# Optimization experiments

Measured on AMD Instinct MI355X. Metric: run time of the kernel, lower is better.

## Reference

```python
import jax, jax.numpy as jnp
import numpy as np

N_NODES = 100000
N_EDGES = 600000
N_GRAPHS = 64


def _segment_mean(x, seg_ids, num_segments):
    s = jax.ops.segment_sum(x, seg_ids, num_segments=num_segments)
    cnt = jax.ops.segment_sum(jnp.ones((x.shape[0],), x.dtype), seg_ids, num_segments=num_segments)
    return s / jnp.maximum(cnt, 1.0)[:, None]


def _sage_conv(x, src, dst, W_l, W_r, b):
    # PyG SAGEConv (mean aggr): out = lin_l(mean_{j->i} x_j) + lin_r(x_i)
    mean_nb = _segment_mean(x[src], dst, x.shape[0])  # [N, d_in]
    return mean_nb @ W_l.T + x @ W_r.T + b


def setup_inputs() -> dict:
    key = jax.random.key(0)
    ks = jax.random.split(key, 16)
    bert_cls = jax.random.normal(ks[0], (N_GRAPHS, 768), jnp.float32)
    node_x = jax.random.normal(ks[1], (N_NODES, 128), jnp.float32)
    edge_index = jax.random.randint(ks[2], (2, N_EDGES), 0, N_NODES, jnp.int64 if jax.config.jax_enable_x64 else jnp.int32)
    batch_ids = jnp.sort(jax.random.randint(ks[3], (N_NODES,), 0, N_GRAPHS))
    s = 0.05
    return {
        'bert_cls': bert_cls,
        'node_x': node_x,
        'edge_index': edge_index,
        'batch_ids': batch_ids,
        'W_adapt': jax.random.normal(ks[4], (64, 768), jnp.float32) * s,
        'b_adapt': jnp.zeros((64,), jnp.float32),
        'W1l': jax.random.normal(ks[5], (64, 128), jnp.float32) * s,
        'W1r': jax.random.normal(ks[6], (64, 128), jnp.float32) * s,
        'b1': jnp.zeros((64,), jnp.float32),
        'W2l': jax.random.normal(ks[7], (16, 64), jnp.float32) * s,
        'W2r': jax.random.normal(ks[8], (16, 64), jnp.float32) * s,
        'b2': jnp.zeros((16,), jnp.float32),
        'Wm': jax.random.normal(ks[9], (16, 16), jnp.float32) * s,
        'bm': jnp.zeros((16,), jnp.float32),
    }


def reference(bert_cls, node_x, edge_index, batch_ids,
              W_adapt, b_adapt, W1l, W1r, b1, W2l, W2r, b2, Wm, bm):
    # pooled BERT CLS -> adaptive linear (forward() applies no relu here)
    last_state = bert_cls @ W_adapt.T + b_adapt  # [bs, 64]

    src, dst = edge_index[0], edge_index[1]
    h = jax.nn.relu(_sage_conv(node_x, src, dst, W1l, W1r, b1))  # [N, 64]
    h = _sage_conv(h, src, dst, W2l, W2r, b2)                    # [N, 16]

    graph_emb = _segment_mean(h, batch_ids, N_GRAPHS)            # [bs, 16]
    graph_emb = graph_emb @ Wm.T + bm

    return jnp.concatenate([last_state, graph_emb], axis=-1)     # [bs, 80]
```

## Files before the change

kernel.cpp:

```cpp
#include <hip/hip_runtime.h>

#define N_NODES 100000
#define N_EDGES 600000
#define N_GRAPHS 64


__global__ void k_count(const int* __restrict__ dst, int* __restrict__ deg) {
    int e = blockIdx.x * 256 + threadIdx.x;
    if (e < N_EDGES) atomicAdd(&deg[dst[e]], 1);
}

__global__ void k_scan1(const int* __restrict__ deg, int* __restrict__ offs,
                        int* __restrict__ bsums) {
    __shared__ int s[256];
    int t = threadIdx.x, b = blockIdx.x;
    int base = b * 1024 + t * 4;
    int v0 = (base + 0 < N_NODES) ? deg[base + 0] : 0;
    int v1 = (base + 1 < N_NODES) ? deg[base + 1] : 0;
    int v2 = (base + 2 < N_NODES) ? deg[base + 2] : 0;
    int v3 = (base + 3 < N_NODES) ? deg[base + 3] : 0;
    int tsum = v0 + v1 + v2 + v3;
    s[t] = tsum;
    __syncthreads();
    for (int o = 1; o < 256; o <<= 1) {
        int x = (t >= o) ? s[t - o] : 0;
        __syncthreads();
        s[t] += x;
        __syncthreads();
    }
    int p = s[t] - tsum;
    if (base + 0 < N_NODES) offs[base + 0] = p;
    p += v0;
    if (base + 1 < N_NODES) offs[base + 1] = p;
    p += v1;
    if (base + 2 < N_NODES) offs[base + 2] = p;
    p += v2;
    if (base + 3 < N_NODES) offs[base + 3] = p;
    if (t == 255) bsums[b] = s[255];
}

__global__ void k_scan2(const int* __restrict__ bsums, int* __restrict__ boff) {
    __shared__ int s[128];
    int t = threadIdx.x;
    int nb = (N_NODES + 1023) / 1024;
    int v = (t < nb) ? bsums[t] : 0;
    s[t] = v;
    __syncthreads();
    for (int o = 1; o < 128; o <<= 1) {
        int x = (t >= o) ? s[t - o] : 0;
        __syncthreads();
        s[t] += x;
        __syncthreads();
    }
    boff[t] = s[t] - v;
}

__global__ void k_scan3(int* __restrict__ offs, const int* __restrict__ boff,
                        int* __restrict__ cursor) {
    int i = blockIdx.x * 256 + threadIdx.x;
    if (i < N_NODES) {
        int v = offs[i] + boff[i >> 10];
        offs[i] = v;
        cursor[i] = v;
    }
}

__global__ void k_fill(const int* __restrict__ src, const int* __restrict__ dst,
                       int* __restrict__ cursor, int* __restrict__ ssrc) {
    int e = blockIdx.x * 256 + threadIdx.x;
    if (e < N_EDGES) {
        int d = dst[e];
        int pos = atomicAdd(&cursor[d], 1);
        ssrc[pos] = src[e];
    }
}

__global__ void k_prepack(const float* __restrict__ W1l, const float* __restrict__ W1r,
                          const float* __restrict__ W2l, const float* __restrict__ W2r,
                          float* __restrict__ Pg, float2* __restrict__ P2) {
    int i = blockIdx.x * 256 + threadIdx.x;
    if (i < 16384) {
        int k = i >> 7, d = i & 127;
        Pg[i] = (d < 64) ? W1l[d * 128 + k] : W1r[(d - 64) * 128 + k];
    } else if (i < 16896) {
        int j = i - 16384, m = j >> 4, d = j & 15;
        P2[j] = make_float2(W2l[d * 64 + 2 * m], W2l[d * 64 + 2 * m + 1]);
    } else if (i < 17408) {
        int j = i - 16896, m = j >> 4, d = j & 15;
        P2[512 + j] = make_float2(W2r[d * 64 + 2 * m], W2r[d * 64 + 2 * m + 1]);
    }
}


#define KC 32
#define LDP 132

__launch_bounds__(256, 4)
__global__ void k_xform1(const float* __restrict__ x, const float* __restrict__ Pg,
                         float* __restrict__ xl, float* __restrict__ xr) {
    __shared__ float At[KC * LDP];
    __shared__ float Bt[KC * LDP];
    int tid = threadIdx.x;
    int wave = tid >> 6, lane = tid & 63;
    int wr = wave >> 1, wc = wave & 1;
    int li = lane >> 3, lj = lane & 7;
    int tbase = blockIdx.x * 128;
    const float4* x4 = (const float4*)x;
    const float4* Pg4 = (const float4*)Pg;

    float acc[8][8];
#pragma unroll
    for (int i = 0; i < 8; ++i)
#pragma unroll
        for (int j = 0; j < 8; ++j) acc[i][j] = 0.f;

    for (int k0 = 0; k0 < 128; k0 += KC) {
        if (k0) __syncthreads();
#pragma unroll
        for (int u = 0; u < 4; ++u) {
            int idx = u * 256 + tid;
            int n = idx >> 3, q = idx & 7;
            int node = min(tbase + n, N_NODES - 1);
            float4 v = x4[node * 32 + (k0 >> 2) + q];
            At[(4 * q + 0) * LDP + n] = v.x;
            At[(4 * q + 1) * LDP + n] = v.y;
            At[(4 * q + 2) * LDP + n] = v.z;
            At[(4 * q + 3) * LDP + n] = v.w;
        }
#pragma unroll
        for (int u = 0; u < 4; ++u) {
            int idx = u * 256 + tid;
            int kk = idx >> 5, q = idx & 31;
            float4 w = Pg4[(k0 + kk) * 32 + q];
            *(float4*)&Bt[kk * LDP + 4 * q] = w;
        }
        __syncthreads();
#pragma unroll 4
        for (int kk = 0; kk < KC; ++kk) {
            float a[8], b[8];
            *(float4*)&a[0] = *(const float4*)&At[kk * LDP + wr * 64 + li * 8];
            *(float4*)&a[4] = *(const float4*)&At[kk * LDP + wr * 64 + li * 8 + 4];
            *(float4*)&b[0] = *(const float4*)&Bt[kk * LDP + wc * 64 + lj * 8];
            *(float4*)&b[4] = *(const float4*)&Bt[kk * LDP + wc * 64 + lj * 8 + 4];
#pragma unroll
            for (int i = 0; i < 8; ++i)
#pragma unroll
                for (int j = 0; j < 8; ++j)
                    acc[i][j] = fmaf(a[i], b[j], acc[i][j]);
        }
    }
    float* outb = wc ? xr : xl;
#pragma unroll
    for (int i = 0; i < 8; ++i) {
        int node = tbase + wr * 64 + li * 8 + i;
        if (node < N_NODES) {
            float4* p = (float4*)(outb + node * 64 + lj * 8);
            p[0] = make_float4(acc[i][0], acc[i][1], acc[i][2], acc[i][3]);
            p[1] = make_float4(acc[i][4], acc[i][5], acc[i][6], acc[i][7]);
        }
    }
}


__launch_bounds__(256)
__global__ void k_gather1(const float* __restrict__ xl, const int* __restrict__ ssrc,
                          const int* __restrict__ offs, const int* __restrict__ deg,
                          const float* __restrict__ b1, float* __restrict__ h1) {
    int tid = blockIdx.x * 256 + threadIdx.x;
    int wid = tid >> 6, lane = tid & 63;
    int nWaves = (gridDim.x * 256) >> 6;
    float bias = b1[lane];

    for (int node = wid; node < N_NODES; node += nWaves) {
        int o  = __builtin_amdgcn_readfirstlane(offs[node]);
        int dg = __builtin_amdgcn_readfirstlane(deg[node]);
        float self = h1[node * 64 + lane];
        float a0 = 0.f, a1 = 0.f, a2 = 0.f, a3 = 0.f;
        int last = dg - 1;
        for (int u = 0; u < dg; u += 4) {
            int n0 = ssrc[o + u];
            int n1 = ssrc[o + min(u + 1, last)];
            int n2 = ssrc[o + min(u + 2, last)];
            int n3 = ssrc[o + min(u + 3, last)];
            float v0 = xl[n0 * 64 + lane];
            float v1 = xl[n1 * 64 + lane];
            float v2 = xl[n2 * 64 + lane];
            float v3 = xl[n3 * 64 + lane];
            float m1 = (u + 1 < dg) ? 1.f : 0.f;
            float m2 = (u + 2 < dg) ? 1.f : 0.f;
            float m3 = (u + 3 < dg) ? 1.f : 0.f;
            a0 += v0;
            a1 = fmaf(v1, m1, a1);
            a2 = fmaf(v2, m2, a2);
            a3 = fmaf(v3, m3, a3);
        }
        float inv = 1.f / (float)max(dg, 1);
        h1[node * 64 + lane] = fmaxf(self + bias + ((a0 + a1) + (a2 + a3)) * inv, 0.f);
    }
}


__launch_bounds__(256)
__global__ void k_xform2(const float* __restrict__ h1,
                         const float2* __restrict__ Pl, const float2* __restrict__ Pr,
                         float* __restrict__ h1l, float* __restrict__ h2pre) {
    __shared__ float2 S[64 * 32];
    int tid = threadIdx.x;
    int wave = __builtin_amdgcn_readfirstlane(tid >> 6);
    int lane = tid & 63;
    int tbase = blockIdx.x * 64;
    const float4* h4 = (const float4*)h1;

    for (int idx = tid; idx < 64 * 16; idx += 256) {
        int n = idx >> 4, m4 = idx & 15;
        if (tbase + n < N_NODES) {
            float4 v = h4[(tbase + n) * 16 + m4];
            int swz = n & 31;
            S[n * 32 + ((2 * m4) ^ swz)]     = make_float2(v.x, v.y);
            S[n * 32 + ((2 * m4 + 1) ^ swz)] = make_float2(v.z, v.w);
        }
    }
    __syncthreads();

    int node = tbase + lane;
    int dbase = wave * 4;
    float accl[4] = {0.f, 0.f, 0.f, 0.f};
    float accr[4] = {0.f, 0.f, 0.f, 0.f};
    int swz = lane & 31;
    const float2* Sn = S + lane * 32;
#pragma unroll 4
    for (int m = 0; m < 32; ++m) {
        float2 s = Sn[m ^ swz];
        const float2* Wl = Pl + m * 16 + dbase;
        const float2* Wr = Pr + m * 16 + dbase;
#pragma unroll
        for (int dd = 0; dd < 4; ++dd) {
            accl[dd] = fmaf(Wl[dd].x, s.x, fmaf(Wl[dd].y, s.y, accl[dd]));
            accr[dd] = fmaf(Wr[dd].x, s.x, fmaf(Wr[dd].y, s.y, accr[dd]));
        }
    }
    if (node < N_NODES) {
        *(float4*)(h1l + node * 16 + dbase)   = make_float4(accl[0], accl[1], accl[2], accl[3]);
        *(float4*)(h2pre + node * 16 + dbase) = make_float4(accr[0], accr[1], accr[2], accr[3]);
    }
}


__launch_bounds__(256)
__global__ void k_g2pool(const float* __restrict__ h1l, const float* __restrict__ h2pre,
                         const int* __restrict__ ssrc, const int* __restrict__ offs,
                         const int* __restrict__ deg, const int* __restrict__ batch,
                         const float* __restrict__ b2,
                         float* __restrict__ gsum, float* __restrict__ gcnt) {
    __shared__ float bins[N_GRAPHS][17];
    int tid = threadIdx.x;
    for (int i = tid; i < N_GRAPHS * 17; i += 256) ((float*)bins)[i] = 0.f;
    __syncthreads();

    int wave = tid >> 6, lane = tid & 63;
    int sub = lane >> 4, d = lane & 15;
    float bias = b2[d];

    int chunk = (N_NODES + gridDim.x - 1) / gridDim.x;
    int cs = blockIdx.x * chunk;
    int ce = min(N_NODES, cs + chunk);

    for (int base = cs + wave * 4; base < ce; base += 16) {
        int node = base + sub;
        bool valid = node < ce;
        int nn = valid ? node : cs;
        int o = offs[nn], dg = deg[nn];
        float a0 = 0.f, a1 = 0.f, a2 = 0.f, a3 = 0.f;
        int last = dg - 1;
        for (int u = 0; u < dg; u += 4) {
            int n0 = ssrc[o + u];
            int n1 = ssrc[o + min(u + 1, last)];
            int n2 = ssrc[o + min(u + 2, last)];
            int n3 = ssrc[o + min(u + 3, last)];
            float v0 = h1l[n0 * 16 + d];
            float v1 = h1l[n1 * 16 + d];
            float v2 = h1l[n2 * 16 + d];
            float v3 = h1l[n3 * 16 + d];
            float m1 = (u + 1 < dg) ? 1.f : 0.f;
            float m2 = (u + 2 < dg) ? 1.f : 0.f;
            float m3 = (u + 3 < dg) ? 1.f : 0.f;
            a0 += v0;
            a1 = fmaf(v1, m1, a1);
            a2 = fmaf(v2, m2, a2);
            a3 = fmaf(v3, m3, a3);
        }
        float inv = 1.f / (float)max(dg, 1);
        float val = h2pre[nn * 16 + d] + bias + ((a0 + a1) + (a2 + a3)) * inv;
        if (valid) {
            int g = batch[nn];
            atomicAdd(&bins[g][d], val);
            if (d == 0) atomicAdd(&bins[g][16], 1.f);
        }
    }
    __syncthreads();
    for (int i = tid; i < N_GRAPHS * 17; i += 256) {
        int g = i / 17, c = i - g * 17;
        float v = bins[g][c];
        if (v != 0.f) {
            if (c < 16) atomicAdd(&gsum[g * 16 + c], v);
            else        atomicAdd(&gcnt[g], v);
        }
    }
}


__global__ void k_final(const float* __restrict__ bert, const float* __restrict__ Wad,
                        const float* __restrict__ bad, const float* __restrict__ Wm,
                        const float* __restrict__ bm, const float* __restrict__ gsum,
                        const float* __restrict__ gcnt, float* __restrict__ out) {
    int g = blockIdx.x;
    int t = threadIdx.x;
    if (t < 64) {
        const float4* br = (const float4*)(bert + g * 768);
        const float4* wr = (const float4*)(Wad + t * 768);
        float acc = bad[t];
#pragma unroll 8
        for (int k = 0; k < 192; ++k) {
            float4 bv = br[k], wv = wr[k];
            acc += bv.x * wv.x + bv.y * wv.y + bv.z * wv.z + bv.w * wv.w;
        }
        out[g * 80 + t] = acc;
    } else if (t < 80) {
        int j = t - 64;
        float ic = 1.f / fmaxf(gcnt[g], 1.f);
        float acc = bm[j];
#pragma unroll
        for (int k = 0; k < 16; ++k) acc += Wm[j * 16 + k] * gsum[g * 16 + k] * ic;
        out[g * 80 + t] = acc;
    }
}

extern "C" void kernel_launch(void* const* d_in, const int* in_sizes, int n_in,
                              void* d_out, int out_size, void* d_ws, size_t ws_size,
                              hipStream_t stream) {
    const float* bert   = (const float*)d_in[0];
    const float* node_x = (const float*)d_in[1];
    const int*   edge   = (const int*)d_in[2];
    const int*   batch  = (const int*)d_in[3];
    const float* Wad    = (const float*)d_in[4];
    const float* bad    = (const float*)d_in[5];
    const float* W1l    = (const float*)d_in[6];
    const float* W1r    = (const float*)d_in[7];
    const float* b1     = (const float*)d_in[8];
    const float* W2l    = (const float*)d_in[9];
    const float* W2r    = (const float*)d_in[10];
    const float* b2     = (const float*)d_in[11];
    const float* Wm     = (const float*)d_in[12];
    const float* bm     = (const float*)d_in[13];
    float* out = (float*)d_out;

    const int* src = edge;
    const int* dst = edge + N_EDGES;

    char* ws = (char*)d_ws;
    int*    deg    = (int*)(ws);
    int*    offs   = (int*)(ws + 400000);
    int*    cursor = (int*)(ws + 800000);
    int*    bsums  = (int*)(ws + 1200000);
    int*    boff   = (int*)(ws + 1200512);
    int*    ssrc   = (int*)(ws + 1201024);
    float*  xl     = (float*)(ws + 3601024);
    float*  h1     = (float*)(ws + 29201024);
    float*  Pg     = (float*)(ws + 54801024);
    float2* P2     = (float2*)(ws + 54866560);
    float*  gsum   = (float*)(ws + 54874752);
    float*  gcnt   = (float*)(ws + 54878848);
    float*  h1l    = (float*)(ws + 3601024);
    float*  h2pre  = (float*)(ws + 10001024);

    float2* P2l = P2;
    float2* P2r = P2 + 512;

    hipMemsetAsync(deg, 0, 400000, stream);
    hipMemsetAsync(gsum, 0, 4096 + 256, stream);

    k_count<<<(N_EDGES + 255) / 256, 256, 0, stream>>>(dst, deg);
    k_scan1<<<(N_NODES + 1023) / 1024, 256, 0, stream>>>(deg, offs, bsums);
    k_scan2<<<1, 128, 0, stream>>>(bsums, boff);
    k_scan3<<<(N_NODES + 255) / 256, 256, 0, stream>>>(offs, boff, cursor);
    k_fill<<<(N_EDGES + 255) / 256, 256, 0, stream>>>(src, dst, cursor, ssrc);
    k_prepack<<<68, 256, 0, stream>>>(W1l, W1r, W2l, W2r, Pg, P2);

    int nT128 = (N_NODES + 127) / 128;
    int nT64  = (N_NODES + 63) / 64;
    k_xform1<<<nT128, 256, 0, stream>>>(node_x, Pg, xl, h1);
    k_gather1<<<2048, 256, 0, stream>>>(xl, ssrc, offs, deg, b1, h1);
    k_xform2<<<nT64, 256, 0, stream>>>(h1, P2l, P2r, h1l, h2pre);
    k_g2pool<<<512, 256, 0, stream>>>(h1l, h2pre, ssrc, offs, deg, batch, b2, gsum, gcnt);
    k_final<<<N_GRAPHS, 128, 0, stream>>>(bert, Wad, bad, Wm, bm, gsum, gcnt, out);
}
```

Before: 325.2 us.

## Prefetch GEMM tiles, swizzle LDS, unroll gather by 8, restructure layer-2 transform

```diff
diff --git a/kernel.cpp b/kernel.cpp
--- a/kernel.cpp
+++ b/kernel.cpp
@@ -77,17 +77,14 @@
 
 __global__ void k_prepack(const float* __restrict__ W1l, const float* __restrict__ W1r,
                           const float* __restrict__ W2l, const float* __restrict__ W2r,
-                          float* __restrict__ Pg, float2* __restrict__ P2) {
+                          float* __restrict__ Pg, float* __restrict__ P2g) {
     int i = blockIdx.x * 256 + threadIdx.x;
     if (i < 16384) {
         int k = i >> 7, d = i & 127;
         Pg[i] = (d < 64) ? W1l[d * 128 + k] : W1r[(d - 64) * 128 + k];
-    } else if (i < 16896) {
-        int j = i - 16384, m = j >> 4, d = j & 15;
-        P2[j] = make_float2(W2l[d * 64 + 2 * m], W2l[d * 64 + 2 * m + 1]);
-    } else if (i < 17408) {
-        int j = i - 16896, m = j >> 4, d = j & 15;
-        P2[512 + j] = make_float2(W2r[d * 64 + 2 * m], W2r[d * 64 + 2 * m + 1]);
+    } else if (i < 18432) {
+        int j = i - 16384, k = j >> 5, d = j & 31;
+        P2g[j] = (d < 16) ? W2l[d * 64 + k] : W2r[(d - 16) * 64 + k];
     }
 }
 
@@ -108,6 +105,15 @@
     const float4* x4 = (const float4*)x;
     const float4* Pg4 = (const float4*)Pg;
 
+    float4 av[4], bv[4];
+#pragma unroll
+    for (int u = 0; u < 4; ++u) {
+        int idx = u * 256 + tid;
+        int n = idx >> 3, q = idx & 7;
+        int node = min(tbase + n, N_NODES - 1);
+        av[u] = x4[node * 32 + q];
+        bv[u] = Pg4[idx];
+    }
     float acc[8][8];
 #pragma unroll
     for (int i = 0; i < 8; ++i)
@@ -115,31 +121,35 @@
         for (int j = 0; j < 8; ++j) acc[i][j] = 0.f;
 
     for (int k0 = 0; k0 < 128; k0 += KC) {
-        if (k0) __syncthreads();
 #pragma unroll
         for (int u = 0; u < 4; ++u) {
             int idx = u * 256 + tid;
             int n = idx >> 3, q = idx & 7;
-            int node = min(tbase + n, N_NODES - 1);
-            float4 v = x4[node * 32 + (k0 >> 2) + q];
-            At[(4 * q + 0) * LDP + n] = v.x;
-            At[(4 * q + 1) * LDP + n] = v.y;
-            At[(4 * q + 2) * LDP + n] = v.z;
-            At[(4 * q + 3) * LDP + n] = v.w;
-        }
-#pragma unroll
-        for (int u = 0; u < 4; ++u) {
-            int idx = u * 256 + tid;
-            int kk = idx >> 5, q = idx & 31;
-            float4 w = Pg4[(k0 + kk) * 32 + q];
-            *(float4*)&Bt[kk * LDP + 4 * q] = w;
-        }
-        __syncthreads();
+            int ns = n ^ ((q & 7) << 3);
+            At[(4 * q + 0) * LDP + ns] = av[u].x;
+            At[(4 * q + 1) * LDP + ns] = av[u].y;
+            At[(4 * q + 2) * LDP + ns] = av[u].z;
+            At[(4 * q + 3) * LDP + ns] = av[u].w;
+            int kk = idx >> 5, q2 = idx & 31;
+            *(float4*)&Bt[kk * LDP + 4 * q2] = bv[u];
+        }
+        __syncthreads();
+        if (k0 + KC < 128) {
+#pragma unroll
+            for (int u = 0; u < 4; ++u) {
+                int idx = u * 256 + tid;
+                int n = idx >> 3, q = idx & 7;
+                int node = min(tbase + n, N_NODES - 1);
+                av[u] = x4[node * 32 + ((k0 + KC) >> 2) + q];
+                bv[u] = Pg4[(k0 + KC) * 32 + idx];
+            }
+        }
 #pragma unroll 4
         for (int kk = 0; kk < KC; ++kk) {
             float a[8], b[8];
-            *(float4*)&a[0] = *(const float4*)&At[kk * LDP + wr * 64 + li * 8];
-            *(float4*)&a[4] = *(const float4*)&At[kk * LDP + wr * 64 + li * 8 + 4];
+            int lia = (li ^ ((kk >> 2) & 7)) * 8;
+            *(float4*)&a[0] = *(const float4*)&At[kk * LDP + wr * 64 + lia];
+            *(float4*)&a[4] = *(const float4*)&At[kk * LDP + wr * 64 + lia + 4];
             *(float4*)&b[0] = *(const float4*)&Bt[kk * LDP + wc * 64 + lj * 8];
             *(float4*)&b[4] = *(const float4*)&Bt[kk * LDP + wc * 64 + lj * 8 + 4];
 #pragma unroll
@@ -148,6 +158,7 @@
                 for (int j = 0; j < 8; ++j)
                     acc[i][j] = fmaf(a[i], b[j], acc[i][j]);
         }
+        __syncthreads();
     }
     float* outb = wc ? xr : xl;
 #pragma unroll
@@ -171,40 +182,68 @@
     int nWaves = (gridDim.x * 256) >> 6;
     float bias = b1[lane];
 
-    for (int node = wid; node < N_NODES; node += nWaves) {
-        int o  = __builtin_amdgcn_readfirstlane(offs[node]);
-        int dg = __builtin_amdgcn_readfirstlane(deg[node]);
-        float self = h1[node * 64 + lane];
+    int node = wid;
+    if (node >= N_NODES) return;
+    int o = offs[node], dg = deg[node];
+    float self = h1[node * 64 + lane];
+    while (true) {
+        int nnode = node + nWaves;
+        int no = 0, ndg = 0;
+        float nself = 0.f;
+        if (nnode < N_NODES) {
+            no = offs[nnode];
+            ndg = deg[nnode];
+            nself = h1[nnode * 64 + lane];
+        }
+        int os = __builtin_amdgcn_readfirstlane(o);
+        int ds = __builtin_amdgcn_readfirstlane(dg);
         float a0 = 0.f, a1 = 0.f, a2 = 0.f, a3 = 0.f;
-        int last = dg - 1;
-        for (int u = 0; u < dg; u += 4) {
-            int n0 = ssrc[o + u];
-            int n1 = ssrc[o + min(u + 1, last)];
-            int n2 = ssrc[o + min(u + 2, last)];
-            int n3 = ssrc[o + min(u + 3, last)];
+        float a4 = 0.f, a5 = 0.f, a6 = 0.f, a7 = 0.f;
+        int last = ds - 1;
+        for (int u = 0; u < ds; u += 8) {
+            int n0 = ssrc[os + u];
+            int n1 = ssrc[os + min(u + 1, last)];
+            int n2 = ssrc[os + min(u + 2, last)];
+            int n3 = ssrc[os + min(u + 3, last)];
+            int n4 = ssrc[os + min(u + 4, last)];
+            int n5 = ssrc[os + min(u + 5, last)];
+            int n6 = ssrc[os + min(u + 6, last)];
+            int n7 = ssrc[os + min(u + 7, last)];
             float v0 = xl[n0 * 64 + lane];
             float v1 = xl[n1 * 64 + lane];
             float v2 = xl[n2 * 64 + lane];
             float v3 = xl[n3 * 64 + lane];
-            float m1 = (u + 1 < dg) ? 1.f : 0.f;
-            float m2 = (u + 2 < dg) ? 1.f : 0.f;
-            float m3 = (u + 3 < dg) ? 1.f : 0.f;
+            float v4 = xl[n4 * 64 + lane];
+            float v5 = xl[n5 * 64 + lane];
+            float v6 = xl[n6 * 64 + lane];
+            float v7 = xl[n7 * 64 + lane];
             a0 += v0;
-            a1 = fmaf(v1, m1, a1);
-            a2 = fmaf(v2, m2, a2);
-            a3 = fmaf(v3, m3, a3);
-        }
-        float inv = 1.f / (float)max(dg, 1);
-        h1[node * 64 + lane] = fmaxf(self + bias + ((a0 + a1) + (a2 + a3)) * inv, 0.f);
-    }
-}
-
+            a1 = fmaf(v1, (u + 1 < ds) ? 1.f : 0.f, a1);
+            a2 = fmaf(v2, (u + 2 < ds) ? 1.f : 0.f, a2);
+            a3 = fmaf(v3, (u + 3 < ds) ? 1.f : 0.f, a3);
+            a4 = fmaf(v4, (u + 4 < ds) ? 1.f : 0.f, a4);
+            a5 = fmaf(v5, (u + 5 < ds) ? 1.f : 0.f, a5);
+            a6 = fmaf(v6, (u + 6 < ds) ? 1.f : 0.f, a6);
+            a7 = fmaf(v7, (u + 7 < ds) ? 1.f : 0.f, a7);
+        }
+        float inv = 1.f / (float)max(ds, 1);
+        float mean = (((a0 + a1) + (a2 + a3)) + ((a4 + a5) + (a6 + a7))) * inv;
+        h1[node * 64 + lane] = fmaxf(self + bias + mean, 0.f);
+        if (nnode >= N_NODES) break;
+        node = nnode;
+        o = no;
+        dg = ndg;
+        self = nself;
+    }
+}
+
+
+#define LD2 68
 
 __launch_bounds__(256)
-__global__ void k_xform2(const float* __restrict__ h1,
-                         const float2* __restrict__ Pl, const float2* __restrict__ Pr,
+__global__ void k_xform2(const float* __restrict__ h1, const float* __restrict__ P2g,
                          float* __restrict__ h1l, float* __restrict__ h2pre) {
-    __shared__ float2 S[64 * 32];
+    __shared__ float S[64 * LD2];
     int tid = threadIdx.x;
     int wave = __builtin_amdgcn_readfirstlane(tid >> 6);
     int lane = tid & 63;
@@ -212,36 +251,41 @@
     const float4* h4 = (const float4*)h1;
 
     for (int idx = tid; idx < 64 * 16; idx += 256) {
-        int n = idx >> 4, m4 = idx & 15;
-        if (tbase + n < N_NODES) {
-            float4 v = h4[(tbase + n) * 16 + m4];
-            int swz = n & 31;
-            S[n * 32 + ((2 * m4) ^ swz)]     = make_float2(v.x, v.y);
-            S[n * 32 + ((2 * m4 + 1) ^ swz)] = make_float2(v.z, v.w);
-        }
+        int n = idx >> 4, q = idx & 15;
+        int node = min(tbase + n, N_NODES - 1);
+        *(float4*)&S[n * LD2 + 4 * q] = h4[node * 16 + q];
     }
     __syncthreads();
 
     int node = tbase + lane;
-    int dbase = wave * 4;
-    float accl[4] = {0.f, 0.f, 0.f, 0.f};
-    float accr[4] = {0.f, 0.f, 0.f, 0.f};
-    int swz = lane & 31;
-    const float2* Sn = S + lane * 32;
+    int dbase = wave * 8;
+    float acc[8] = {0.f, 0.f, 0.f, 0.f, 0.f, 0.f, 0.f, 0.f};
+    const float* Sn = S + lane * LD2;
 #pragma unroll 4
-    for (int m = 0; m < 32; ++m) {
-        float2 s = Sn[m ^ swz];
-        const float2* Wl = Pl + m * 16 + dbase;
-        const float2* Wr = Pr + m * 16 + dbase;
-#pragma unroll
-        for (int dd = 0; dd < 4; ++dd) {
-            accl[dd] = fmaf(Wl[dd].x, s.x, fmaf(Wl[dd].y, s.y, accl[dd]));
-            accr[dd] = fmaf(Wr[dd].x, s.x, fmaf(Wr[dd].y, s.y, accr[dd]));
+    for (int k4 = 0; k4 < 16; ++k4) {
+        float4 s = *(const float4*)&Sn[4 * k4];
+        const float* Wk = P2g + (4 * k4) * 32 + dbase;
+#pragma unroll
+        for (int c = 0; c < 4; ++c) {
+            float sv = (c == 0) ? s.x : (c == 1) ? s.y : (c == 2) ? s.z : s.w;
+            const float* W = Wk + c * 32;
+#pragma unroll
+            for (int dd = 0; dd < 8; ++dd)
+                acc[dd] = fmaf(W[dd], sv, acc[dd]);
         }
     }
     if (node < N_NODES) {
-        *(float4*)(h1l + node * 16 + dbase)   = make_float4(accl[0], accl[1], accl[2], accl[3]);
-        *(float4*)(h2pre + node * 16 + dbase) = make_float4(accr[0], accr[1], accr[2], accr[3]);
+        float4 lo = make_float4(acc[0], acc[1], acc[2], acc[3]);
+        float4 hi = make_float4(acc[4], acc[5], acc[6], acc[7]);
+        if (wave < 2) {
+            float4* p = (float4*)(h1l + node * 16 + wave * 8);
+            p[0] = lo;
+            p[1] = hi;
+        } else {
+            float4* p = (float4*)(h2pre + node * 16 + (wave - 2) * 8);
+            p[0] = lo;
+            p[1] = hi;
+        }
     }
 }
 
@@ -367,14 +411,11 @@
     float*  xl     = (float*)(ws + 3601024);
     float*  h1     = (float*)(ws + 29201024);
     float*  Pg     = (float*)(ws + 54801024);
-    float2* P2     = (float2*)(ws + 54866560);
+    float*  P2g    = (float*)(ws + 54866560);
     float*  gsum   = (float*)(ws + 54874752);
     float*  gcnt   = (float*)(ws + 54878848);
     float*  h1l    = (float*)(ws + 3601024);
     float*  h2pre  = (float*)(ws + 10001024);
-
-    float2* P2l = P2;
-    float2* P2r = P2 + 512;
 
     hipMemsetAsync(deg, 0, 400000, stream);
     hipMemsetAsync(gsum, 0, 4096 + 256, stream);
@@ -384,13 +425,13 @@
     k_scan2<<<1, 128, 0, stream>>>(bsums, boff);
     k_scan3<<<(N_NODES + 255) / 256, 256, 0, stream>>>(offs, boff, cursor);
     k_fill<<<(N_EDGES + 255) / 256, 256, 0, stream>>>(src, dst, cursor, ssrc);
-    k_prepack<<<68, 256, 0, stream>>>(W1l, W1r, W2l, W2r, Pg, P2);
+    k_prepack<<<72, 256, 0, stream>>>(W1l, W1r, W2l, W2r, Pg, P2g);
 
     int nT128 = (N_NODES + 127) / 128;
     int nT64  = (N_NODES + 63) / 64;
     k_xform1<<<nT128, 256, 0, stream>>>(node_x, Pg, xl, h1);
     k_gather1<<<2048, 256, 0, stream>>>(xl, ssrc, offs, deg, b1, h1);
-    k_xform2<<<nT64, 256, 0, stream>>>(h1, P2l, P2r, h1l, h2pre);
+    k_xform2<<<nT64, 256, 0, stream>>>(h1, P2g, h1l, h2pre);
     k_g2pool<<<512, 256, 0, stream>>>(h1l, h2pre, ssrc, offs, deg, batch, b2, gsum, gcnt);
     k_final<<<N_GRAPHS, 128, 0, stream>>>(bert, Wad, bad, Wm, bm, gsum, gcnt, out);
 }
```

After: 334.4 us. 1.03x slower.
